# Performance work log

Measured on AMD Instinct MI355X. Metric: run time of the kernel, lower is better.

The kernel has to match this reference:

```python
import jax, jax.numpy as jnp
import numpy as np

EPS = 1e-5
B, T, D, H = 4096, 256, 36, 64


def setup_inputs() -> dict:
    key = jax.random.key(0)
    ks = jax.random.split(key, 24)
    f32 = jnp.float32
    u = lambda k, shape, s: jax.random.uniform(k, shape, f32, -s, s)
    sH = 1.0 / np.sqrt(H)   # GRUCell / Linear(in=64) init scale
    sD = 1.0 / np.sqrt(D)
    sC = 1.0 / np.sqrt(2 * D)  # combine Linear(72,36)
    return {
        "values": jax.random.normal(ks[0], (B, T, D), f32),
        "masks": (jax.random.uniform(ks[1], (B, T, D)) > 0.2).astype(f32),
        "deltas": jax.random.uniform(ks[2], (B, T, D), f32) * 5.0,
        "label": (jax.random.uniform(ks[3], (B,)) > 0.5).astype(f32),
        "is_train": jnp.ones((B,), f32),
        # GRUCell(108, 64): gate order r, z, n (PyTorch convention)
        "W_ih": u(ks[4], (3 * H, 3 * D), sH),
        "W_hh": u(ks[5], (3 * H, H), sH),
        "b_ih": u(ks[6], (3 * H,), sH),
        "b_hh": u(ks[7], (3 * H,), sH),
        "hist_W": u(ks[8], (1, H), sH),
        "hist_b": u(ks[9], (1,), sH),
        "feat_W": u(ks[10], (D, D), sD),
        "feat_b": u(ks[11], (D,), sD),
        "decay_W": u(ks[12], (D, D), sD),
        "decay_b": u(ks[13], (D,), sD),
        "comb_W": u(ks[14], (D, 2 * D), sC),
        "comb_b": u(ks[15], (D,), sC),
        "out_W": u(ks[16], (1, H), sH),
        "out_b": u(ks[17], (1,), sH),
    }


def reference(values, masks, deltas, label, is_train,
              W_ih, W_hh, b_ih, b_hh, hist_W, hist_b,
              feat_W, feat_b, decay_W, decay_b,
              comb_W, comb_b, out_W, out_b):
    feat_Wm = feat_W * (1.0 - jnp.eye(D, dtype=feat_W.dtype))  # zero diagonal

    def step(carry, xs):
        h, h_sum, il = carry
        value, mask, delta = xs  # each [B, D]
        msum = jnp.sum(mask) + EPS
        value_x = h @ hist_W.T + hist_b                      # [B, 1], broadcasts
        il = il + jnp.sum(jnp.abs(value_x - value) * mask) / msum
        value_c = mask * value + (1.0 - mask) * value_x
        gamma = jnp.exp(-jax.nn.relu(delta @ decay_W.T + decay_b))
        beta = jax.nn.sigmoid(jnp.concatenate([gamma, mask], axis=1) @ comb_W.T + comb_b)
        value_z = value_c @ feat_Wm.T + feat_b
        il = il + jnp.sum(jnp.abs(value_z - value) * mask) / msum
        value_h = value_z * beta + value_x * (1.0 - beta)
        il = il + jnp.sum(jnp.abs(value_h - value) * mask) / msum
        value_c = mask * value + (1.0 - mask) * value_h
        x = jnp.concatenate([value_c, mask, gamma], axis=1)  # [B, 3D]
        gi = x @ W_ih.T + b_ih
        gh = h @ W_hh.T + b_hh
        i_r, i_z, i_n = jnp.split(gi, 3, axis=1)
        h_r, h_z, h_n = jnp.split(gh, 3, axis=1)
        r = jax.nn.sigmoid(i_r + h_r)
        z = jax.nn.sigmoid(i_z + h_z)
        n = jnp.tanh(i_n + r * h_n)
        h_new = (1.0 - z) * n + z * h
        return (h_new, h_sum + h_new, il), value_c

    init = (jnp.zeros((B, H), values.dtype),
            jnp.zeros((B, H), values.dtype),
            jnp.zeros((), values.dtype))
    xs = (values.transpose(1, 0, 2), masks.transpose(1, 0, 2), deltas.transpose(1, 0, 2))
    (h, h_sum, impute_loss), imp = jax.lax.scan(step, init, xs)

    impute_loss = impute_loss / T
    h_sum = h_sum / T
    logits = h_sum @ out_W.T + out_b                          # [B, 1]
    y = label.reshape(-1, 1)
    w = is_train.reshape(-1, 1)
    # binary_cross_entropy_with_logits, reduce=False
    bce = jnp.maximum(logits, 0.0) - logits * y + jnp.log1p(jnp.exp(-jnp.abs(logits)))
    class_loss = jnp.sum(bce * w) / (jnp.sum(w) + EPS)
    loss = class_loss + impute_loss  # alpha = 1.0
    pred = jax.nn.sigmoid(logits)
    impute_values = imp.transpose(1, 0, 2).reshape(B, T * D)  # concat over time on dim 1
    return loss, impute_values, pred
```

## Files before the change

kernel.cpp:

```cpp
#include <hip/hip_runtime.h>
#include <hip/hip_bf16.h>


#define Bsz 4096
#define Tn  256
#define Dn  36
#define ROWS 16
#define EPSf 1e-5f
#define VMST 38

using f32x4 = __attribute__((ext_vector_type(4))) float;
using s8    = __attribute__((ext_vector_type(8))) short;

__device__ __forceinline__ short f2bf(float x) {
  return (short)__bfloat16_as_ushort(__float2bfloat16(x));
}
__device__ __forceinline__ float sigf(float x) { return 1.f / (1.f + __expf(-x)); }
__device__ __forceinline__ float tanhfast(float x) { return 1.f - 2.f / (1.f + __expf(2.f * x)); }
__device__ __forceinline__ int fragoff(int row, int k) {
  return ((k >> 5) << 9) + (((k >> 3) & 3) << 7) + (row << 3) + (k & 7);
}
__device__ __forceinline__ float selq(f32x4 v, int s) {
  float a = (s & 1) ? v[1] : v[0];
  float b = (s & 1) ? v[3] : v[2];
  return (s & 2) ? b : a;
}
#define MFMA __builtin_amdgcn_mfma_f32_16x16x32_bf16

__global__ void msum_k(const float4* __restrict__ masks4, float* __restrict__ rmsum) {
  int t = blockIdx.x;
  float s = 0.f;
  for (int r = threadIdx.x; r < Bsz; r += 256) {
    const float4* mp = masks4 + ((size_t)r * Tn + t) * 9;
    #pragma unroll
    for (int j = 0; j < 9; ++j) { float4 v = mp[j]; s += v.x + v.y + v.z + v.w; }
  }
  __shared__ float red[256];
  red[threadIdx.x] = s;
  __syncthreads();
  for (int k = 128; k > 0; k >>= 1) {
    if (threadIdx.x < k) red[threadIdx.x] += red[threadIdx.x + k];
    __syncthreads();
  }
  if (threadIdx.x == 0) rmsum[t] = 1.f / (red[0] + EPSf);
}

__global__ __launch_bounds__(512) void brits_main(
    const float* __restrict__ values, const float* __restrict__ masks,
    const float* __restrict__ deltas, const float* __restrict__ label,
    const float* __restrict__ is_train,
    const float* __restrict__ W_ih, const float* __restrict__ W_hh,
    const float* __restrict__ b_ih, const float* __restrict__ b_hh,
    const float* __restrict__ hist_W, const float* __restrict__ hist_b,
    const float* __restrict__ feat_W, const float* __restrict__ feat_b,
    const float* __restrict__ decay_W, const float* __restrict__ decay_b,
    const float* __restrict__ comb_W, const float* __restrict__ comb_b,
    const float* __restrict__ out_W, const float* __restrict__ out_b,
    float* __restrict__ out, const float* __restrict__ rmsum,
    float* __restrict__ ws_acc ) {

  __shared__ __align__(16) float2 vm_s[2][ROWS * VMST];
  __shared__ __align__(16) short hbuf[1024];
  __shared__ __align__(16) short dbuf[2][1024];
  __shared__ __align__(16) short xbuf[2][2048];
  __shared__ __align__(16) short vcbuf[4][1024];
  __shared__ __align__(16) short cxbuf[4][1536];
  __shared__ __align__(16) short whh_l[24 * 512];
  __shared__ __align__(16) short comb_l[9 * 512];
  __shared__ float red16[16];

  const int tid  = threadIdx.x;
  const int w    = tid >> 6;
  const int lane = tid & 63;
  const int lc   = lane & 15;
  const int r4   = lane >> 4;
  const int row0 = blockIdx.x * ROWS;
  const int k0b  = r4 * 8;
  const int lw8  = lane * 8;

  const bool isG = (w < 4);
  const int  sW  = isG ? 0 : (w - 4);
  const int  dim = 16 * (isG ? w : 0) + lc;
  const int  myrow = 4 * r4 + sW;

  s8 bf[14];
  #pragma unroll
  for (int i = 0; i < 14; ++i) bf[i] = (s8)(short)0;

  if (isG) {
    #pragma unroll
    for (int g = 0; g < 3; ++g) {
      const int n = 64 * g + dim;
      #pragma unroll
      for (int kt = 0; kt < 4; ++kt) {
        s8 f;
        #pragma unroll
        for (int e = 0; e < 8; ++e) {
          int xk = k0b + 32 * kt + e;
          float wv = 0.f;
          if (xk < 72) wv = W_ih[n * 108 + 36 + xk];
          else if (xk < 108) wv = W_ih[n * 108 + xk - 72];
          f[e] = f2bf(wv);
        }
        bf[g * 4 + kt] = f;
      }
      #pragma unroll
      for (int kt = 0; kt < 2; ++kt) {
        s8 f;
        #pragma unroll
        for (int e = 0; e < 8; ++e) f[e] = f2bf(W_hh[n * 64 + k0b + 32 * kt + e]);
        *(s8*)&whh_l[(w * 6 + g * 2 + kt) * 512 + lw8] = f;
      }
    }
  } else {
    #pragma unroll
    for (int t3 = 0; t3 < 3; ++t3) {
      const int col = 16 * t3 + lc;
      const bool cok = (col < Dn);
      #pragma unroll
      for (int kt = 0; kt < 2; ++kt) {
        s8 fd, ff;
        #pragma unroll
        for (int e = 0; e < 8; ++e) {
          int k = k0b + 32 * kt + e;
          fd[e] = f2bf((cok && k < Dn) ? decay_W[col * Dn + k] : 0.f);
          ff[e] = f2bf((cok && k < Dn && k != col) ? feat_W[col * Dn + k] : 0.f);
        }
        bf[t3 * 2 + kt] = fd;
        bf[6 + t3 * 2 + kt] = ff;
      }
    }
    #pragma unroll
    for (int kt = 0; kt < 2; ++kt) {
      s8 f;
      #pragma unroll
      for (int e = 0; e < 8; ++e) f[e] = f2bf(hist_W[k0b + 32 * kt + e]);
      bf[12 + kt] = f;
    }
    if (w == 4) {
      #pragma unroll
      for (int t3 = 0; t3 < 3; ++t3) {
        const int col = 16 * t3 + lc;
        const bool cok = (col < Dn);
        #pragma unroll
        for (int kt = 0; kt < 3; ++kt) {
          s8 f;
          #pragma unroll
          for (int e = 0; e < 8; ++e) {
            int k = k0b + 32 * kt + e;
            f[e] = f2bf((cok && k < 72) ? comb_W[col * 72 + k] : 0.f);
          }
          *(s8*)&comb_l[(t3 * 3 + kt) * 512 + lw8] = f;
        }
      }
    }
  }

  float db3[3] = {0,0,0}, fb3[3] = {0,0,0}, cb3[3] = {0,0,0};
  float br = 0.f, bz = 0.f, bin_ = 0.f, bhn = 0.f, ow = 0.f;
  if (isG) {
    br   = b_ih[dim] + b_hh[dim];
    bz   = b_ih[64 + dim] + b_hh[64 + dim];
    bin_ = b_ih[128 + dim];
    bhn  = b_hh[128 + dim];
    ow   = out_W[dim];
  } else {
    #pragma unroll
    for (int t3 = 0; t3 < 3; ++t3) {
      int col = 16 * t3 + lc;
      if (col < Dn) { db3[t3] = decay_b[col]; fb3[t3] = feat_b[col]; cb3[t3] = comb_b[col]; }
    }
  }
  const float histb = hist_b[0];
  const int hb = fragoff(0, dim);

  const bool stg = (tid < 144);
  const int srow = tid / 9;
  const int squad = tid - srow * 9;
  const size_t sbase = ((size_t)(row0 + srow) * Tn) * Dn + squad * 4;
  const int sfo = fragoff(srow, squad * 4);
  const int svo = srow * VMST + squad * 4;

  const int mrow = 4 * (lane / 9) + sW;
  const int mc0  = (lane % 9) * 4;

  for (int i = tid; i < 1024; i += 512) {
    hbuf[i] = 0; dbuf[0][i] = 0; dbuf[1][i] = 0;
    vcbuf[0][i] = 0; vcbuf[1][i] = 0; vcbuf[2][i] = 0; vcbuf[3][i] = 0;
  }
  for (int i = tid; i < 2048; i += 512) { xbuf[0][i] = 0; xbuf[1][i] = 0; }
  for (int i = tid; i < 1536; i += 512) {
    cxbuf[0][i] = 0; cxbuf[1][i] = 0; cxbuf[2][i] = 0; cxbuf[3][i] = 0;
  }
  __syncthreads();

  float4 pv = {0,0,0,0}, pm = {0,0,0,0}, pd = {0,0,0,0};
  if (stg) {
    float4 v0 = *(const float4*)&values[sbase];
    float4 m0 = *(const float4*)&masks[sbase];
    float4 d0 = *(const float4*)&deltas[sbase];
    *(float4*)&vm_s[0][svo]     = make_float4(v0.x, m0.x, v0.y, m0.y);
    *(float4*)&vm_s[0][svo + 2] = make_float4(v0.z, m0.z, v0.w, m0.w);
    union { short s[4]; uint2 u; } td, tm;
    td.s[0]=f2bf(d0.x); td.s[1]=f2bf(d0.y); td.s[2]=f2bf(d0.z); td.s[3]=f2bf(d0.w);
    tm.s[0]=f2bf(m0.x); tm.s[1]=f2bf(m0.y); tm.s[2]=f2bf(m0.z); tm.s[3]=f2bf(m0.w);
    *(uint2*)&dbuf[0][sfo] = td.u;
    *(uint2*)&xbuf[0][sfo] = tm.u;
    pv = *(const float4*)&values[sbase + Dn];
    pm = *(const float4*)&masks[sbase + Dn];
    pd = *(const float4*)&deltas[sbase + Dn];
  }
  __syncthreads();

  float bq[3] = {0.f, 0.f, 0.f};
  if (!isG) {
    s8 ad0 = *(const s8*)&dbuf[0][lw8];
    s8 ad1 = *(const s8*)&dbuf[0][512 + lw8];
    f32x4 G0 = {0,0,0,0}, G1 = {0,0,0,0}, G2 = {0,0,0,0};
    G0 = MFMA(ad0, bf[0], G0, 0,0,0); G0 = MFMA(ad1, bf[1], G0, 0,0,0);
    G1 = MFMA(ad0, bf[2], G1, 0,0,0); G1 = MFMA(ad1, bf[3], G1, 0,0,0);
    G2 = MFMA(ad0, bf[4], G2, 0,0,0); G2 = MFMA(ad1, bf[5], G2, 0,0,0);
    #pragma unroll
    for (int t3 = 0; t3 < 3; ++t3) {
      int col = 16 * t3 + lc;
      if (col < Dn) {
        float gm = (t3==0) ? selq(G0,sW) : (t3==1) ? selq(G1,sW) : selq(G2,sW);
        short gbv = f2bf(__expf(-fmaxf(gm + db3[t3], 0.f)));
        xbuf[0][fragoff(myrow, 36 + col)] = gbv;
        cxbuf[sW][fragoff(myrow, col)] = gbv;
      }
    }
    if (lane < 36) {
      #pragma unroll
      for (int j = 0; j < 4; ++j)
        cxbuf[sW][fragoff(mrow, 36 + mc0 + j)] = f2bf(vm_s[0][mrow * VMST + mc0 + j].y);
    }
    s8 ac0 = *(const s8*)&cxbuf[sW][lw8];
    s8 ac1 = *(const s8*)&cxbuf[sW][512 + lw8];
    s8 ac2 = *(const s8*)&cxbuf[sW][1024 + lw8];
    f32x4 B0 = {0,0,0,0}, B1 = {0,0,0,0}, B2 = {0,0,0,0};
    B0 = MFMA(ac0, *(const s8*)&comb_l[0*512+lw8], B0, 0,0,0);
    B0 = MFMA(ac1, *(const s8*)&comb_l[1*512+lw8], B0, 0,0,0);
    B0 = MFMA(ac2, *(const s8*)&comb_l[2*512+lw8], B0, 0,0,0);
    B1 = MFMA(ac0, *(const s8*)&comb_l[3*512+lw8], B1, 0,0,0);
    B1 = MFMA(ac1, *(const s8*)&comb_l[4*512+lw8], B1, 0,0,0);
    B1 = MFMA(ac2, *(const s8*)&comb_l[5*512+lw8], B1, 0,0,0);
    B2 = MFMA(ac0, *(const s8*)&comb_l[6*512+lw8], B2, 0,0,0);
    B2 = MFMA(ac1, *(const s8*)&comb_l[7*512+lw8], B2, 0,0,0);
    B2 = MFMA(ac2, *(const s8*)&comb_l[8*512+lw8], B2, 0,0,0);
    bq[0] = sigf(selq(B0,sW) + cb3[0]);
    bq[1] = sigf(selq(B1,sW) + cb3[1]);
    bq[2] = sigf(selq(B2,sW) + cb3[2]);
  }

  float hreg[4] = {0.f, 0.f, 0.f, 0.f};
  float lacc[4] = {0.f, 0.f, 0.f, 0.f};
  float il = 0.f;
  __syncthreads();

  #pragma unroll 1
  for (int t = 0; t < Tn; ++t) {
    const float srm = rmsum[t];
    const int p = t & 1;
    f32x4 A0 = {0,0,0,0}, A1 = {0,0,0,0}, A2 = {0,0,0,0}, A3 = {0,0,0,0};

    if (isG) {
      const int wb = w * 6 * 512;
      s8 ah0 = *(const s8*)&hbuf[lw8];
      s8 ah1 = *(const s8*)&hbuf[512 + lw8];
      A0 = MFMA(ah0, *(const s8*)&whh_l[wb + lw8],        A0, 0,0,0);
      A0 = MFMA(ah1, *(const s8*)&whh_l[wb + 512 + lw8],  A0, 0,0,0);
      A1 = MFMA(ah0, *(const s8*)&whh_l[wb + 1024 + lw8], A1, 0,0,0);
      A1 = MFMA(ah1, *(const s8*)&whh_l[wb + 1536 + lw8], A1, 0,0,0);
      A3 = MFMA(ah0, *(const s8*)&whh_l[wb + 2048 + lw8], A3, 0,0,0);
      A3 = MFMA(ah1, *(const s8*)&whh_l[wb + 2560 + lw8], A3, 0,0,0);
      s8 ax0 = *(const s8*)&xbuf[p][lw8];
      s8 ax1 = *(const s8*)&xbuf[p][512 + lw8];
      A0 = MFMA(ax0, bf[0], A0, 0,0,0); A0 = MFMA(ax1, bf[1], A0, 0,0,0);
      A1 = MFMA(ax0, bf[4], A1, 0,0,0); A1 = MFMA(ax1, bf[5], A1, 0,0,0);
      A2 = MFMA(ax0, bf[8], A2, 0,0,0); A2 = MFMA(ax1, bf[9], A2, 0,0,0);
      if (stg && t + 1 < Tn) {
        *(float4*)&vm_s[p ^ 1][svo]     = make_float4(pv.x, pm.x, pv.y, pm.y);
        *(float4*)&vm_s[p ^ 1][svo + 2] = make_float4(pv.z, pm.z, pv.w, pm.w);
        union { short s[4]; uint2 u; } td, tm;
        td.s[0]=f2bf(pd.x); td.s[1]=f2bf(pd.y); td.s[2]=f2bf(pd.z); td.s[3]=f2bf(pd.w);
        tm.s[0]=f2bf(pm.x); tm.s[1]=f2bf(pm.y); tm.s[2]=f2bf(pm.z); tm.s[3]=f2bf(pm.w);
        *(uint2*)&dbuf[p ^ 1][sfo] = td.u;
        *(uint2*)&xbuf[p ^ 1][sfo] = tm.u;
      }
      if (stg && t + 2 < Tn) {
        size_t o = sbase + (size_t)(t + 2) * Dn;
        pv = *(const float4*)&values[o];
        pm = *(const float4*)&masks[o];
        pd = *(const float4*)&deltas[o];
      }
    } else {
      s8 ah0 = *(const s8*)&hbuf[lw8];
      s8 ah1 = *(const s8*)&hbuf[512 + lw8];
      f32x4 X = {0,0,0,0};
      X = MFMA(ah0, bf[12], X, 0,0,0);
      X = MFMA(ah1, bf[13], X, 0,0,0);
      const float vx = selq(X, sW) + histb;
      float v3[3], m3[3];
      #pragma unroll
      for (int t3 = 0; t3 < 3; ++t3) {
        int col = 16 * t3 + lc;
        v3[t3] = 0.f; m3[t3] = 0.f;
        if (col < Dn) {
          float2 vm = vm_s[p][myrow * VMST + col];
          v3[t3] = vm.x; m3[t3] = vm.y;
          il += srm * fabsf(vx - vm.x) * vm.y;
          vcbuf[sW][fragoff(myrow, col)] = f2bf(vm.y * vm.x + (1.f - vm.y) * vx);
        }
      }
      s8 av0 = *(const s8*)&vcbuf[sW][lw8];
      s8 av1 = *(const s8*)&vcbuf[sW][512 + lw8];
      f32x4 Z0 = {0,0,0,0}, Z1 = {0,0,0,0}, Z2 = {0,0,0,0};
      Z0 = MFMA(av0, bf[6],  Z0, 0,0,0); Z0 = MFMA(av1, bf[7],  Z0, 0,0,0);
      Z1 = MFMA(av0, bf[8],  Z1, 0,0,0); Z1 = MFMA(av1, bf[9],  Z1, 0,0,0);
      Z2 = MFMA(av0, bf[10], Z2, 0,0,0); Z2 = MFMA(av1, bf[11], Z2, 0,0,0);
      #pragma unroll
      for (int t3 = 0; t3 < 3; ++t3) {
        int col = 16 * t3 + lc;
        if (col < Dn) {
          float vz = ((t3==0) ? selq(Z0,sW) : (t3==1) ? selq(Z1,sW) : selq(Z2,sW)) + fb3[t3];
          il += srm * fabsf(vz - v3[t3]) * m3[t3];
          float vh = vz * bq[t3] + vx * (1.f - bq[t3]);
          il += srm * fabsf(vh - v3[t3]) * m3[t3];
          float vc2 = m3[t3] * v3[t3] + (1.f - m3[t3]) * vh;
          out[1 + ((size_t)(row0 + myrow) * Tn + t) * Dn + col] = vc2;
          xbuf[p][fragoff(myrow, 72 + col)] = f2bf(vc2);
        }
      }
    }
    __syncthreads();

    if (isG) {
      s8 ax2 = *(const s8*)&xbuf[p][1024 + lw8];
      s8 ax3 = *(const s8*)&xbuf[p][1536 + lw8];
      A0 = MFMA(ax2, bf[2],  A0, 0,0,0); A0 = MFMA(ax3, bf[3],  A0, 0,0,0);
      A1 = MFMA(ax2, bf[6],  A1, 0,0,0); A1 = MFMA(ax3, bf[7],  A1, 0,0,0);
      A2 = MFMA(ax2, bf[10], A2, 0,0,0); A2 = MFMA(ax3, bf[11], A2, 0,0,0);
      #pragma unroll
      for (int q = 0; q < 4; ++q) {
        float rg = sigf(A0[q] + br);
        float zg = sigf(A1[q] + bz);
        float ng = tanhfast(A2[q] + bin_ + rg * (A3[q] + bhn));
        float hn = (1.f - zg) * ng + zg * hreg[q];
        hreg[q] = hn;
        lacc[q] += hn * ow;
        hbuf[hb + (r4 * 4 + q) * 8] = f2bf(hn);
      }
    } else if (t + 1 < Tn) {
      s8 ad0 = *(const s8*)&dbuf[p ^ 1][lw8];
      s8 ad1 = *(const s8*)&dbuf[p ^ 1][512 + lw8];
      f32x4 G0 = {0,0,0,0}, G1 = {0,0,0,0}, G2 = {0,0,0,0};
      G0 = MFMA(ad0, bf[0], G0, 0,0,0); G0 = MFMA(ad1, bf[1], G0, 0,0,0);
      G1 = MFMA(ad0, bf[2], G1, 0,0,0); G1 = MFMA(ad1, bf[3], G1, 0,0,0);
      G2 = MFMA(ad0, bf[4], G2, 0,0,0); G2 = MFMA(ad1, bf[5], G2, 0,0,0);
      #pragma unroll
      for (int t3 = 0; t3 < 3; ++t3) {
        int col = 16 * t3 + lc;
        if (col < Dn) {
          float gm = (t3==0) ? selq(G0,sW) : (t3==1) ? selq(G1,sW) : selq(G2,sW);
          short gbv = f2bf(__expf(-fmaxf(gm + db3[t3], 0.f)));
          xbuf[p ^ 1][fragoff(myrow, 36 + col)] = gbv;
          cxbuf[sW][fragoff(myrow, col)] = gbv;
        }
      }
      if (lane < 36) {
        #pragma unroll
        for (int j = 0; j < 4; ++j)
          cxbuf[sW][fragoff(mrow, 36 + mc0 + j)] =
              f2bf(vm_s[p ^ 1][mrow * VMST + mc0 + j].y);
      }
      s8 ac0 = *(const s8*)&cxbuf[sW][lw8];
      s8 ac1 = *(const s8*)&cxbuf[sW][512 + lw8];
      s8 ac2 = *(const s8*)&cxbuf[sW][1024 + lw8];
      f32x4 B0 = {0,0,0,0}, B1 = {0,0,0,0}, B2 = {0,0,0,0};
      B0 = MFMA(ac0, *(const s8*)&comb_l[0*512+lw8], B0, 0,0,0);
      B0 = MFMA(ac1, *(const s8*)&comb_l[1*512+lw8], B0, 0,0,0);
      B0 = MFMA(ac2, *(const s8*)&comb_l[2*512+lw8], B0, 0,0,0);
      B1 = MFMA(ac0, *(const s8*)&comb_l[3*512+lw8], B1, 0,0,0);
      B1 = MFMA(ac1, *(const s8*)&comb_l[4*512+lw8], B1, 0,0,0);
      B1 = MFMA(ac2, *(const s8*)&comb_l[5*512+lw8], B1, 0,0,0);
      B2 = MFMA(ac0, *(const s8*)&comb_l[6*512+lw8], B2, 0,0,0);
      B2 = MFMA(ac1, *(const s8*)&comb_l[7*512+lw8], B2, 0,0,0);
      B2 = MFMA(ac2, *(const s8*)&comb_l[8*512+lw8], B2, 0,0,0);
      bq[0] = sigf(selq(B0,sW) + cb3[0]);
      bq[1] = sigf(selq(B1,sW) + cb3[1]);
      bq[2] = sigf(selq(B2,sW) + cb3[2]);
    }
    __syncthreads();
  }

  float* red_s = (float*)whh_l;
  red_s[tid] = il;
  __syncthreads();
  for (int k = 256; k > 0; k >>= 1) {
    if (tid < k) red_s[tid] += red_s[tid + k];
    __syncthreads();
  }
  if (tid == 0) atomicAdd(&ws_acc[0], red_s[0]);
  if (tid < 16) red16[tid] = 0.f;
  __syncthreads();
  if (isG) {
    #pragma unroll
    for (int q = 0; q < 4; ++q) atomicAdd(&red16[r4 * 4 + q], lacc[q]);
  }
  __syncthreads();

  if (tid < ROWS) {
    float lg = red16[tid] / (float)Tn + out_b[0];
    int rg = row0 + tid;
    float pred = sigf(lg);
    out[1 + (size_t)Bsz * Tn * Dn + rg] = pred;
    float y = label[rg], wt = is_train[rg];
    float bce = fmaxf(lg, 0.f) - lg * y + log1pf(__expf(-fabsf(lg)));
    atomicAdd(&ws_acc[1], bce * wt);
    atomicAdd(&ws_acc[2], wt);
  }
}

__global__ void fin_k(const float* __restrict__ ws, float* __restrict__ out) {
  out[0] = ws[1] / (ws[2] + EPSf) + ws[0] / (float)Tn;
}

extern "C" void kernel_launch(void* const* d_in, const int* in_sizes, int n_in,
                              void* d_out, int out_size, void* d_ws, size_t ws_size,
                              hipStream_t stream) {
  const float* values   = (const float*)d_in[0];
  const float* masks    = (const float*)d_in[1];
  const float* deltas   = (const float*)d_in[2];
  const float* label    = (const float*)d_in[3];
  const float* is_train = (const float*)d_in[4];
  const float* W_ih     = (const float*)d_in[5];
  const float* W_hh     = (const float*)d_in[6];
  const float* b_ih     = (const float*)d_in[7];
  const float* b_hh     = (const float*)d_in[8];
  const float* hist_W   = (const float*)d_in[9];
  const float* hist_b   = (const float*)d_in[10];
  const float* feat_W   = (const float*)d_in[11];
  const float* feat_b   = (const float*)d_in[12];
  const float* decay_W  = (const float*)d_in[13];
  const float* decay_b  = (const float*)d_in[14];
  const float* comb_W   = (const float*)d_in[15];
  const float* comb_b   = (const float*)d_in[16];
  const float* out_W    = (const float*)d_in[17];
  const float* out_b    = (const float*)d_in[18];

  float* ws = (float*)d_ws;
  float* rmsum = ws + 4;
  float* out = (float*)d_out;

  hipMemsetAsync(d_ws, 0, 16, stream);
  msum_k<<<Tn, 256, 0, stream>>>((const float4*)masks, rmsum);
  brits_main<<<Bsz / ROWS, 512, 0, stream>>>(
      values, masks, deltas, label, is_train, W_ih, W_hh, b_ih, b_hh,
      hist_W, hist_b, feat_W, feat_b, decay_W, decay_b, comb_W, comb_b,
      out_W, out_b, out, rmsum, ws);
  fin_k<<<1, 1, 0, stream>>>(ws, out);
}
```

Before: 509.3 us.

## Keep W_hh and comb_W fragments in registers and reuse xbuf as comb input

```diff
diff --git a/kernel.cpp b/kernel.cpp
--- a/kernel.cpp
+++ b/kernel.cpp
@@ -64,9 +64,7 @@
   __shared__ __align__(16) short dbuf[2][1024];
   __shared__ __align__(16) short xbuf[2][2048];
   __shared__ __align__(16) short vcbuf[4][1024];
-  __shared__ __align__(16) short cxbuf[4][1536];
-  __shared__ __align__(16) short whh_l[24 * 512];
-  __shared__ __align__(16) short comb_l[9 * 512];
+  __shared__ float red_s[512];
   __shared__ float red16[16];
 
   const int tid  = threadIdx.x;
@@ -83,9 +81,9 @@
   const int  dim = 16 * (isG ? w : 0) + lc;
   const int  myrow = 4 * r4 + sW;
 
-  s8 bf[14];
+  s8 bf[23];
   #pragma unroll
-  for (int i = 0; i < 14; ++i) bf[i] = (s8)(short)0;
+  for (int i = 0; i < 23; ++i) bf[i] = (s8)(short)0;
 
   if (isG) {
     #pragma unroll
@@ -109,7 +107,7 @@
         s8 f;
         #pragma unroll
         for (int e = 0; e < 8; ++e) f[e] = f2bf(W_hh[n * 64 + k0b + 32 * kt + e]);
-        *(s8*)&whh_l[(w * 6 + g * 2 + kt) * 512 + lw8] = f;
+        bf[12 + g * 2 + kt] = f;
       }
     }
   } else {
@@ -129,6 +127,21 @@
         bf[t3 * 2 + kt] = fd;
         bf[6 + t3 * 2 + kt] = ff;
       }
+      #pragma unroll
+      for (int kt = 0; kt < 3; ++kt) {
+        s8 f;
+        #pragma unroll
+        for (int e = 0; e < 8; ++e) {
+          int xk = k0b + 32 * kt + e;
+          float wv = 0.f;
+          if (cok) {
+            if (xk < 36) wv = comb_W[col * 72 + 36 + xk];
+            else if (xk < 72) wv = comb_W[col * 72 + xk - 36];
+          }
+          f[e] = f2bf(wv);
+        }
+        bf[14 + t3 * 3 + kt] = f;
+      }
     }
     #pragma unroll
     for (int kt = 0; kt < 2; ++kt) {
@@ -136,23 +149,6 @@
       #pragma unroll
       for (int e = 0; e < 8; ++e) f[e] = f2bf(hist_W[k0b + 32 * kt + e]);
       bf[12 + kt] = f;
-    }
-    if (w == 4) {
-      #pragma unroll
-      for (int t3 = 0; t3 < 3; ++t3) {
-        const int col = 16 * t3 + lc;
-        const bool cok = (col < Dn);
-        #pragma unroll
-        for (int kt = 0; kt < 3; ++kt) {
-          s8 f;
-          #pragma unroll
-          for (int e = 0; e < 8; ++e) {
-            int k = k0b + 32 * kt + e;
-            f[e] = f2bf((cok && k < 72) ? comb_W[col * 72 + k] : 0.f);
-          }
-          *(s8*)&comb_l[(t3 * 3 + kt) * 512 + lw8] = f;
-        }
-      }
     }
   }
 
@@ -181,17 +177,11 @@
   const int sfo = fragoff(srow, squad * 4);
   const int svo = srow * VMST + squad * 4;
 
-  const int mrow = 4 * (lane / 9) + sW;
-  const int mc0  = (lane % 9) * 4;
-
   for (int i = tid; i < 1024; i += 512) {
     hbuf[i] = 0; dbuf[0][i] = 0; dbuf[1][i] = 0;
     vcbuf[0][i] = 0; vcbuf[1][i] = 0; vcbuf[2][i] = 0; vcbuf[3][i] = 0;
   }
   for (int i = tid; i < 2048; i += 512) { xbuf[0][i] = 0; xbuf[1][i] = 0; }
-  for (int i = tid; i < 1536; i += 512) {
-    cxbuf[0][i] = 0; cxbuf[1][i] = 0; cxbuf[2][i] = 0; cxbuf[3][i] = 0;
-  }
   __syncthreads();
 
   float4 pv = {0,0,0,0}, pm = {0,0,0,0}, pd = {0,0,0,0};
@@ -225,29 +215,19 @@
       int col = 16 * t3 + lc;
       if (col < Dn) {
         float gm = (t3==0) ? selq(G0,sW) : (t3==1) ? selq(G1,sW) : selq(G2,sW);
-        short gbv = f2bf(__expf(-fmaxf(gm + db3[t3], 0.f)));
-        xbuf[0][fragoff(myrow, 36 + col)] = gbv;
-        cxbuf[sW][fragoff(myrow, col)] = gbv;
-      }
-    }
-    if (lane < 36) {
-      #pragma unroll
-      for (int j = 0; j < 4; ++j)
-        cxbuf[sW][fragoff(mrow, 36 + mc0 + j)] = f2bf(vm_s[0][mrow * VMST + mc0 + j].y);
-    }
-    s8 ac0 = *(const s8*)&cxbuf[sW][lw8];
-    s8 ac1 = *(const s8*)&cxbuf[sW][512 + lw8];
-    s8 ac2 = *(const s8*)&cxbuf[sW][1024 + lw8];
+        xbuf[0][fragoff(myrow, 36 + col)] = f2bf(__expf(-fmaxf(gm + db3[t3], 0.f)));
+      }
+    }
+    s8 ac0 = *(const s8*)&xbuf[0][lw8];
+    s8 ac1 = *(const s8*)&xbuf[0][512 + lw8];
+    s8 ac2 = *(const s8*)&xbuf[0][1024 + lw8];
     f32x4 B0 = {0,0,0,0}, B1 = {0,0,0,0}, B2 = {0,0,0,0};
-    B0 = MFMA(ac0, *(const s8*)&comb_l[0*512+lw8], B0, 0,0,0);
-    B0 = MFMA(ac1, *(const s8*)&comb_l[1*512+lw8], B0, 0,0,0);
-    B0 = MFMA(ac2, *(const s8*)&comb_l[2*512+lw8], B0, 0,0,0);
-    B1 = MFMA(ac0, *(const s8*)&comb_l[3*512+lw8], B1, 0,0,0);
-    B1 = MFMA(ac1, *(const s8*)&comb_l[4*512+lw8], B1, 0,0,0);
-    B1 = MFMA(ac2, *(const s8*)&comb_l[5*512+lw8], B1, 0,0,0);
-    B2 = MFMA(ac0, *(const s8*)&comb_l[6*512+lw8], B2, 0,0,0);
-    B2 = MFMA(ac1, *(const s8*)&comb_l[7*512+lw8], B2, 0,0,0);
-    B2 = MFMA(ac2, *(const s8*)&comb_l[8*512+lw8], B2, 0,0,0);
+    B0 = MFMA(ac0, bf[14], B0, 0,0,0); B0 = MFMA(ac1, bf[15], B0, 0,0,0);
+    B0 = MFMA(ac2, bf[16], B0, 0,0,0);
+    B1 = MFMA(ac0, bf[17], B1, 0,0,0); B1 = MFMA(ac1, bf[18], B1, 0,0,0);
+    B1 = MFMA(ac2, bf[19], B1, 0,0,0);
+    B2 = MFMA(ac0, bf[20], B2, 0,0,0); B2 = MFMA(ac1, bf[21], B2, 0,0,0);
+    B2 = MFMA(ac2, bf[22], B2, 0,0,0);
     bq[0] = sigf(selq(B0,sW) + cb3[0]);
     bq[1] = sigf(selq(B1,sW) + cb3[1]);
     bq[2] = sigf(selq(B2,sW) + cb3[2]);
@@ -258,24 +238,23 @@
   float il = 0.f;
   __syncthreads();
 
-  #pragma unroll 1
+  #pragma unroll 2
   for (int t = 0; t < Tn; ++t) {
     const float srm = rmsum[t];
     const int p = t & 1;
+    short* __restrict__ xb  = xbuf[p];
+    short* __restrict__ xb2 = xbuf[p ^ 1];
+    short* __restrict__ db2 = dbuf[p ^ 1];
     f32x4 A0 = {0,0,0,0}, A1 = {0,0,0,0}, A2 = {0,0,0,0}, A3 = {0,0,0,0};
 
     if (isG) {
-      const int wb = w * 6 * 512;
       s8 ah0 = *(const s8*)&hbuf[lw8];
       s8 ah1 = *(const s8*)&hbuf[512 + lw8];
-      A0 = MFMA(ah0, *(const s8*)&whh_l[wb + lw8],        A0, 0,0,0);
-      A0 = MFMA(ah1, *(const s8*)&whh_l[wb + 512 + lw8],  A0, 0,0,0);
-      A1 = MFMA(ah0, *(const s8*)&whh_l[wb + 1024 + lw8], A1, 0,0,0);
-      A1 = MFMA(ah1, *(const s8*)&whh_l[wb + 1536 + lw8], A1, 0,0,0);
-      A3 = MFMA(ah0, *(const s8*)&whh_l[wb + 2048 + lw8], A3, 0,0,0);
-      A3 = MFMA(ah1, *(const s8*)&whh_l[wb + 2560 + lw8], A3, 0,0,0);
-      s8 ax0 = *(const s8*)&xbuf[p][lw8];
-      s8 ax1 = *(const s8*)&xbuf[p][512 + lw8];
+      A0 = MFMA(ah0, bf[12], A0, 0,0,0); A0 = MFMA(ah1, bf[13], A0, 0,0,0);
+      A1 = MFMA(ah0, bf[14], A1, 0,0,0); A1 = MFMA(ah1, bf[15], A1, 0,0,0);
+      A3 = MFMA(ah0, bf[16], A3, 0,0,0); A3 = MFMA(ah1, bf[17], A3, 0,0,0);
+      s8 ax0 = *(const s8*)&xb[lw8];
+      s8 ax1 = *(const s8*)&xb[512 + lw8];
       A0 = MFMA(ax0, bf[0], A0, 0,0,0); A0 = MFMA(ax1, bf[1], A0, 0,0,0);
       A1 = MFMA(ax0, bf[4], A1, 0,0,0); A1 = MFMA(ax1, bf[5], A1, 0,0,0);
       A2 = MFMA(ax0, bf[8], A2, 0,0,0); A2 = MFMA(ax1, bf[9], A2, 0,0,0);
@@ -285,8 +264,8 @@
         union { short s[4]; uint2 u; } td, tm;
         td.s[0]=f2bf(pd.x); td.s[1]=f2bf(pd.y); td.s[2]=f2bf(pd.z); td.s[3]=f2bf(pd.w);
         tm.s[0]=f2bf(pm.x); tm.s[1]=f2bf(pm.y); tm.s[2]=f2bf(pm.z); tm.s[3]=f2bf(pm.w);
-        *(uint2*)&dbuf[p ^ 1][sfo] = td.u;
-        *(uint2*)&xbuf[p ^ 1][sfo] = tm.u;
+        *(uint2*)&db2[sfo] = td.u;
+        *(uint2*)&xb2[sfo] = tm.u;
       }
       if (stg && t + 2 < Tn) {
         size_t o = sbase + (size_t)(t + 2) * Dn;
@@ -329,15 +308,15 @@
           il += srm * fabsf(vh - v3[t3]) * m3[t3];
           float vc2 = m3[t3] * v3[t3] + (1.f - m3[t3]) * vh;
           out[1 + ((size_t)(row0 + myrow) * Tn + t) * Dn + col] = vc2;
-          xbuf[p][fragoff(myrow, 72 + col)] = f2bf(vc2);
+          xb[fragoff(myrow, 72 + col)] = f2bf(vc2);
         }
       }
     }
     __syncthreads();
 
     if (isG) {
-      s8 ax2 = *(const s8*)&xbuf[p][1024 + lw8];
-      s8 ax3 = *(const s8*)&xbuf[p][1536 + lw8];
+      s8 ax2 = *(const s8*)&xb[1024 + lw8];
+      s8 ax3 = *(const s8*)&xb[1536 + lw8];
       A0 = MFMA(ax2, bf[2],  A0, 0,0,0); A0 = MFMA(ax3, bf[3],  A0, 0,0,0);
       A1 = MFMA(ax2, bf[6],  A1, 0,0,0); A1 = MFMA(ax3, bf[7],  A1, 0,0,0);
       A2 = MFMA(ax2, bf[10], A2, 0,0,0); A2 = MFMA(ax3, bf[11], A2, 0,0,0);
@@ -352,8 +331,8 @@
         hbuf[hb + (r4 * 4 + q) * 8] = f2bf(hn);
       }
     } else if (t + 1 < Tn) {
-      s8 ad0 = *(const s8*)&dbuf[p ^ 1][lw8];
-      s8 ad1 = *(const s8*)&dbuf[p ^ 1][512 + lw8];
+      s8 ad0 = *(const s8*)&db2[lw8];
+      s8 ad1 = *(const s8*)&db2[512 + lw8];
       f32x4 G0 = {0,0,0,0}, G1 = {0,0,0,0}, G2 = {0,0,0,0};
       G0 = MFMA(ad0, bf[0], G0, 0,0,0); G0 = MFMA(ad1, bf[1], G0, 0,0,0);
       G1 = MFMA(ad0, bf[2], G1, 0,0,0); G1 = MFMA(ad1, bf[3], G1, 0,0,0);
@@ -363,30 +342,19 @@
         int col = 16 * t3 + lc;
         if (col < Dn) {
           float gm = (t3==0) ? selq(G0,sW) : (t3==1) ? selq(G1,sW) : selq(G2,sW);
-          short gbv = f2bf(__expf(-fmaxf(gm + db3[t3], 0.f)));
-          xbuf[p ^ 1][fragoff(myrow, 36 + col)] = gbv;
-          cxbuf[sW][fragoff(myrow, col)] = gbv;
-        }
-      }
-      if (lane < 36) {
-        #pragma unroll
-        for (int j = 0; j < 4; ++j)
-          cxbuf[sW][fragoff(mrow, 36 + mc0 + j)] =
-              f2bf(vm_s[p ^ 1][mrow * VMST + mc0 + j].y);
-      }
-      s8 ac0 = *(const s8*)&cxbuf[sW][lw8];
-      s8 ac1 = *(const s8*)&cxbuf[sW][512 + lw8];
-      s8 ac2 = *(const s8*)&cxbuf[sW][1024 + lw8];
+          xb2[fragoff(myrow, 36 + col)] = f2bf(__expf(-fmaxf(gm + db3[t3], 0.f)));
+        }
+      }
+      s8 ac0 = *(const s8*)&xb2[lw8];
+      s8 ac1 = *(const s8*)&xb2[512 + lw8];
+      s8 ac2 = *(const s8*)&xb2[1024 + lw8];
       f32x4 B0 = {0,0,0,0}, B1 = {0,0,0,0}, B2 = {0,0,0,0};
-      B0 = MFMA(ac0, *(const s8*)&comb_l[0*512+lw8], B0, 0,0,0);
-      B0 = MFMA(ac1, *(const s8*)&comb_l[1*512+lw8], B0, 0,0,0);
-      B0 = MFMA(ac2, *(const s8*)&comb_l[2*512+lw8], B0, 0,0,0);
-      B1 = MFMA(ac0, *(const s8*)&comb_l[3*512+lw8], B1, 0,0,0);
-      B1 = MFMA(ac1, *(const s8*)&comb_l[4*512+lw8], B1, 0,0,0);
-      B1 = MFMA(ac2, *(const s8*)&comb_l[5*512+lw8], B1, 0,0,0);
-      B2 = MFMA(ac0, *(const s8*)&comb_l[6*512+lw8], B2, 0,0,0);
-      B2 = MFMA(ac1, *(const s8*)&comb_l[7*512+lw8], B2, 0,0,0);
-      B2 = MFMA(ac2, *(const s8*)&comb_l[8*512+lw8], B2, 0,0,0);
+      B0 = MFMA(ac0, bf[14], B0, 0,0,0); B0 = MFMA(ac1, bf[15], B0, 0,0,0);
+      B0 = MFMA(ac2, bf[16], B0, 0,0,0);
+      B1 = MFMA(ac0, bf[17], B1, 0,0,0); B1 = MFMA(ac1, bf[18], B1, 0,0,0);
+      B1 = MFMA(ac2, bf[19], B1, 0,0,0);
+      B2 = MFMA(ac0, bf[20], B2, 0,0,0); B2 = MFMA(ac1, bf[21], B2, 0,0,0);
+      B2 = MFMA(ac2, bf[22], B2, 0,0,0);
       bq[0] = sigf(selq(B0,sW) + cb3[0]);
       bq[1] = sigf(selq(B1,sW) + cb3[1]);
       bq[2] = sigf(selq(B2,sW) + cb3[2]);
@@ -394,7 +362,6 @@
     __syncthreads();
   }
 
-  float* red_s = (float*)whh_l;
   red_s[tid] = il;
   __syncthreads();
   for (int k = 256; k > 0; k >>= 1) {
```

Measured after the change: 458.3 us. 1.11x faster.
